# Kernel optimization log

Hardware: AMD Instinct MI355X
Metric: run time of the kernel (lower is better)

## Reference

```python
import jax, jax.numpy as jnp
import numpy as np
from jax import lax

B, S, D, H, FF, STEPS = 8, 1024, 512, 8, 2048, 64
HD = D // H
EPS = 1e-5
NEG_INF = -1e30


def setup_inputs() -> dict:
    key = jax.random.key(0)
    ks = jax.random.split(key, 8)
    sc = 0.02
    inp = {
        "x": jax.random.normal(ks[0], (B, S, D), jnp.float32),
        "decode_x": jax.random.normal(ks[1], (STEPS, B, 1, D), jnp.float32),
        # bool attn mask, True = masked (future positions), matching the torch code
        "causal_mask": jnp.triu(jnp.ones((S, S), bool), k=1),
        "qkv_w": jax.random.normal(ks[2], (3 * D, D), jnp.float32) * sc,
        "qkv_b": jnp.zeros((3 * D,), jnp.float32),
        "out_w": jax.random.normal(ks[3], (D, D), jnp.float32) * sc,
        "out_b": jnp.zeros((D,), jnp.float32),
        "w1": jax.random.normal(ks[4], (FF, D), jnp.float32) * sc,
        "b1": jnp.zeros((FF,), jnp.float32),
        "w2": jax.random.normal(ks[5], (D, FF), jnp.float32) * sc,
        "b2": jnp.zeros((D,), jnp.float32),
        "ln1_w": jnp.ones((D,), jnp.float32),
        "ln1_b": jnp.zeros((D,), jnp.float32),
        "ln2_w": jnp.ones((D,), jnp.float32),
        "ln2_b": jnp.zeros((D,), jnp.float32),
    }
    return inp


def _layer_norm(x, w, b):
    mu = jnp.mean(x, axis=-1, keepdims=True)
    var = jnp.mean(jnp.square(x - mu), axis=-1, keepdims=True)
    return (x - mu) * lax.rsqrt(var + EPS) * w + b


def _mlp(x, w1, b1, w2, b2):
    h = jax.nn.relu(jnp.einsum("bsd,fd->bsf", x, w1) + b1)
    return jnp.einsum("bsf,df->bsd", h, w2) + b2


def _attend(q, k, v, mask):
    # q:[B,H,L,hd] k,v:[B,H,T,hd] mask broadcastable to [B,H,L,T], True = masked
    scale = 1.0 / np.sqrt(HD)
    scores = jnp.einsum("bhld,bhtd->bhlt", q, k) * scale
    scores = jnp.where(mask, NEG_INF, scores)
    w = jax.nn.softmax(scores, axis=-1)
    w = jnp.where(mask, 0.0, w)  # torch code zeros masked weights post-softmax
    return jnp.einsum("bhlt,bhtd->bhld", w, v)


def _heads(t):  # [B,T,D] -> [B,H,T,hd]
    return t.reshape(t.shape[0], t.shape[1], H, HD).transpose(0, 2, 1, 3)


def reference(x, decode_x, causal_mask, qkv_w, qkv_b, out_w, out_b,
              w1, b1, w2, b2, ln1_w, ln1_b, ln2_w, ln2_b):
    # ---- process_prompt (prefill) ----
    qkv = jnp.einsum("bsd,ed->bse", x, qkv_w) + qkv_b  # [B,S,3D]
    q, k, v = jnp.split(qkv, 3, axis=-1)
    attn = _attend(_heads(q), _heads(k), _heads(v), causal_mask[None, None])
    attn = attn.transpose(0, 2, 1, 3).reshape(B, S, D)
    h = x + (jnp.einsum("bsd,ed->bse", attn, out_w) + out_b)
    h = _layer_norm(h, ln1_w, ln1_b)
    h = h + _mlp(h, w1, b1, w2, b2)
    prefill_out = _layer_norm(h, ln2_w, ln2_b)

    cap = S + STEPS
    k_cache = jnp.zeros((B, cap, D), x.dtype).at[:, :S].set(k)
    v_cache = jnp.zeros((B, cap, D), x.dtype).at[:, :S].set(v)
    pos = jnp.arange(cap)

    def step(carry, x_t):
        k_cache, v_cache, cur_len = carry
        qkv = jnp.einsum("bsd,ed->bse", x_t, qkv_w) + qkv_b  # [B,1,3D]
        q, kk, vv = jnp.split(qkv, 3, axis=-1)
        k_cache = lax.dynamic_update_slice(k_cache, kk, (0, cur_len, 0))
        v_cache = lax.dynamic_update_slice(v_cache, vv, (0, cur_len, 0))
        kv_len = cur_len + 1
        mask = (pos >= kv_len)[None, None, None, :]  # [1,1,1,cap]
        attn = _attend(_heads(q), _heads(k_cache), _heads(v_cache), mask)
        attn = attn.transpose(0, 2, 1, 3).reshape(B, 1, D)
        h = x_t + (jnp.einsum("bsd,ed->bse", attn, out_w) + out_b)
        h = _layer_norm(h, ln1_w, ln1_b)
        h = h + _mlp(h, w1, b1, w2, b2)
        h = _layer_norm(h, ln2_w, ln2_b)
        return (k_cache, v_cache, kv_len), h

    (_, _, _), dec = lax.scan(step, (k_cache, v_cache, jnp.int32(S)), decode_x)
    dec = dec.squeeze(2).transpose(1, 0, 2)  # [B,STEPS,D]
    return jnp.concatenate([prefill_out, dec], axis=1)  # [B,S+STEPS,D]
```

## Files before the change

### kernel.cpp

```cpp
#include <hip/hip_runtime.h>
#include <cstdint>

#define CAP_ 1088
#define EPS_ 1e-5f

using bf8   = __attribute__((ext_vector_type(8))) short;
using f32x4 = __attribute__((ext_vector_type(4))) float;

__device__ __forceinline__ unsigned short f2bf(float f) {
  unsigned u = __float_as_uint(f);
  u += 0x7fffu + ((u >> 16) & 1);
  return (unsigned short)(u >> 16);
}
__device__ __forceinline__ float bf2f(unsigned short v) {
  return __uint_as_float((unsigned)v << 16);
}

typedef const __attribute__((address_space(1))) void* gp1;
typedef __attribute__((address_space(3))) void* lp3;
__device__ __forceinline__ void async16(const void* g, void* l) {
  __builtin_amdgcn_global_load_lds((gp1)g, (lp3)l, 16, 0, 0);
}

__global__ __launch_bounds__(256) void cvt_bf16(const float* __restrict__ in,
                                                unsigned short* __restrict__ out,
                                                int n4) {
  int i = blockIdx.x * 256 + threadIdx.x;
  if (i >= n4) return;
  float4 v = ((const float4*)in)[i];
  ushort4 o;
  o.x = f2bf(v.x); o.y = f2bf(v.y); o.z = f2bf(v.z); o.w = f2bf(v.w);
  ((ushort4*)out)[i] = o;
}

__global__ __launch_bounds__(256) void mfma_gemm(
    const unsigned short* __restrict__ A, const unsigned short* __restrict__ Bw,
    const float* __restrict__ bias,
    unsigned short* __restrict__ Cb,
    unsigned short* __restrict__ kb, unsigned short* __restrict__ vt,
    int M, int N, int K, int mode, int relu)
{
  __shared__ unsigned short Als[128 * 64];
  __shared__ unsigned short Bls[128 * 64];
  const int tid  = threadIdx.x;
  const int lane = tid & 63, w = tid >> 6;
  const int bm = blockIdx.x * 128, bn = blockIdx.y * 128;
  const int wm = (w >> 1) * 64, wn = (w & 1) * 64;

  f32x4 acc[4][4] = {};

  const int so = tid * 16;
  for (int k0 = 0; k0 < K; k0 += 64) {
#pragma unroll
    for (int it = 0; it < 4; ++it) {
      int o   = it * 4096 + so;
      int row = o >> 7;
      int ch  = (o >> 4) & 7;
      int sch = ch ^ (row & 7);
      async16(A  + (size_t)(bm + row) * K + k0 + sch * 8, (char*)Als + o);
      async16(Bw + (size_t)(bn + row) * K + k0 + sch * 8, (char*)Bls + o);
    }
    __syncthreads();
#pragma unroll
    for (int ks = 0; ks < 2; ++ks) {
      bf8 af[4], bfr[4];
#pragma unroll
      for (int m = 0; m < 4; ++m) {
        int row = wm + m * 16 + (lane & 15);
        int ch  = ks * 4 + (lane >> 4);
        af[m] = *(const bf8*)((const char*)Als + row * 128 + ((ch ^ (row & 7)) * 16));
      }
#pragma unroll
      for (int n = 0; n < 4; ++n) {
        int row = wn + n * 16 + (lane & 15);
        int ch  = ks * 4 + (lane >> 4);
        bfr[n] = *(const bf8*)((const char*)Bls + row * 128 + ((ch ^ (row & 7)) * 16));
      }
#pragma unroll
      for (int m = 0; m < 4; ++m)
#pragma unroll
        for (int n = 0; n < 4; ++n)
          acc[m][n] = __builtin_amdgcn_mfma_f32_16x16x32_bf16(af[m], bfr[n], acc[m][n], 0, 0, 0);
    }
    __syncthreads();
  }

#pragma unroll
  for (int m = 0; m < 4; ++m) {
#pragma unroll
    for (int n = 0; n < 4; ++n) {
      int col  = bn + wn + n * 16 + (lane & 15);
      int row0 = bm + wm + m * 16 + ((lane >> 4) << 2);
      float bcol = bias[col];
      if (mode == 1) {
        if (col < 512) {
#pragma unroll
          for (int r = 0; r < 4; ++r)
            Cb[((size_t)(row0 + r) << 9) + col] = f2bf((acc[m][n][r] + bcol) * 0.125f);
        } else if (col < 1024) {
#pragma unroll
          for (int r = 0; r < 4; ++r) {
            int row = row0 + r; int bb, pos;
            if (row < 8192) { bb = row >> 10; pos = row & 1023; }
            else { int r2 = row - 8192; bb = r2 & 7; pos = 1024 + (r2 >> 3); }
            kb[(((size_t)(bb * CAP_ + pos)) << 9) + (col - 512)] = f2bf(acc[m][n][r] + bcol);
          }
        } else {
          int c = col - 1024; int hh = c >> 6, d = c & 63;
          if (row0 < 8192) {
            int bb = row0 >> 10, pos = row0 & 1023;
            ushort4 pk;
            pk.x = f2bf(acc[m][n][0] + bcol); pk.y = f2bf(acc[m][n][1] + bcol);
            pk.z = f2bf(acc[m][n][2] + bcol); pk.w = f2bf(acc[m][n][3] + bcol);
            *(ushort4*)(vt + ((size_t)((bb * 8 + hh) * 64 + d)) * CAP_ + pos) = pk;
          } else {
#pragma unroll
            for (int r = 0; r < 4; ++r) {
              int r2 = row0 + r - 8192; int bb = r2 & 7, pos = 1024 + (r2 >> 3);
              vt[((size_t)((bb * 8 + hh) * 64 + d)) * CAP_ + pos] = f2bf(acc[m][n][r] + bcol);
            }
          }
        }
      } else {
#pragma unroll
        for (int r = 0; r < 4; ++r) {
          float v = acc[m][n][r] + bcol;
          if (relu) v = fmaxf(v, 0.f);
          Cb[(size_t)(row0 + r) * N + col] = f2bf(v);
        }
      }
    }
  }
}

__global__ __launch_bounds__(256) void gemm_fullrow_ln(
    const unsigned short* __restrict__ A,
    const unsigned short* __restrict__ Bw,
    const float* __restrict__ bias,
    const unsigned short* __restrict__ resb,
    const float* __restrict__ lnw, const float* __restrict__ lnb,
    unsigned short* __restrict__ outb, float* __restrict__ outf,
    int K, int mode)
{
  __shared__ unsigned short Bls[512 * 64];
  const int tid = threadIdx.x, lane = tid & 63, w = tid >> 6;
  const int l4 = lane >> 4, l15 = lane & 15;
  const int bm = blockIdx.x * 32;

  f32x4 acc[2][8] = {};
  bf8 a_cur[2][2], a_nxt[2][2];

#pragma unroll
  for (int ks = 0; ks < 2; ++ks)
#pragma unroll
    for (int mf = 0; mf < 2; ++mf)
      a_cur[ks][mf] = *(const bf8*)(A + (size_t)(bm + mf * 16 + l15) * K + (ks * 4 + l4) * 8);

  for (int k0 = 0; k0 < K; k0 += 64) {
#pragma unroll
    for (int it = 0; it < 16; ++it) {
      int o   = it * 4096 + tid * 16;
      int row = o >> 7;
      int sch = ((o >> 4) & 7) ^ (row & 7);
      async16(Bw + (size_t)row * K + k0 + sch * 8, (char*)Bls + o);
    }
    if (k0 + 64 < K) {
#pragma unroll
      for (int ks = 0; ks < 2; ++ks)
#pragma unroll
        for (int mf = 0; mf < 2; ++mf)
          a_nxt[ks][mf] = *(const bf8*)(A + (size_t)(bm + mf * 16 + l15) * K +
                                        k0 + 64 + (ks * 4 + l4) * 8);
    }
    __syncthreads();
#pragma unroll
    for (int ks = 0; ks < 2; ++ks) {
      int cb = ks * 4 + l4;
#pragma unroll
      for (int nf = 0; nf < 8; ++nf) {
        int row = w * 128 + nf * 16 + l15;
        bf8 bfv = *(const bf8*)((const char*)Bls + row * 128 + ((cb ^ (row & 7)) << 4));
#pragma unroll
        for (int mf = 0; mf < 2; ++mf)
          acc[mf][nf] = __builtin_amdgcn_mfma_f32_16x16x32_bf16(a_cur[ks][mf], bfv, acc[mf][nf], 0, 0, 0);
      }
    }
#pragma unroll
    for (int ks = 0; ks < 2; ++ks)
#pragma unroll
      for (int mf = 0; mf < 2; ++mf)
        a_cur[ks][mf] = a_nxt[ks][mf];
    __syncthreads();
  }

  float bc[8], lw[8], lb[8];
#pragma unroll
  for (int nf = 0; nf < 8; ++nf) {
    int col = w * 128 + nf * 16 + l15;
    bc[nf] = bias[col]; lw[nf] = lnw[col]; lb[nf] = lnb[col];
  }
#pragma unroll
  for (int nf = 0; nf < 8; ++nf) {
    int col = w * 128 + nf * 16 + l15;
#pragma unroll
    for (int mf = 0; mf < 2; ++mf)
#pragma unroll
      for (int r = 0; r < 4; ++r) {
        int rowg = bm + mf * 16 + l4 * 4 + r;
        acc[mf][nf][r] += bc[nf] + bf2f(resb[(size_t)rowg * 512 + col]);
      }
  }

  float* red = (float*)Bls;
#pragma unroll
  for (int mf = 0; mf < 2; ++mf)
#pragma unroll
    for (int r = 0; r < 4; ++r) {
      float s = 0.f, q = 0.f;
#pragma unroll
      for (int nf = 0; nf < 8; ++nf) { float v = acc[mf][nf][r]; s += v; q += v * v; }
#pragma unroll
      for (int off = 1; off < 16; off <<= 1) {
        s += __shfl_xor(s, off, 64); q += __shfl_xor(q, off, 64);
      }
      if (l15 == 0) {
        int rl = mf * 16 + l4 * 4 + r;
        red[rl * 8 + w * 2]     = s;
        red[rl * 8 + w * 2 + 1] = q;
      }
    }
  __syncthreads();

#pragma unroll
  for (int mf = 0; mf < 2; ++mf)
#pragma unroll
    for (int r = 0; r < 4; ++r) {
      int rl = mf * 16 + l4 * 4 + r;
      float S = red[rl * 8 + 0] + red[rl * 8 + 2] + red[rl * 8 + 4] + red[rl * 8 + 6];
      float Q = red[rl * 8 + 1] + red[rl * 8 + 3] + red[rl * 8 + 5] + red[rl * 8 + 7];
      float mu  = S * (1.f / 512.f);
      float var = Q * (1.f / 512.f) - mu * mu;
      float inv = rsqrtf(var + EPS_);
      int rowg = bm + rl;
      if (mode == 0) {
#pragma unroll
        for (int nf = 0; nf < 8; ++nf) {
          int col = w * 128 + nf * 16 + l15;
          float y = (acc[mf][nf][r] - mu) * inv * lw[nf] + lb[nf];
          outb[(size_t)rowg * 512 + col] = f2bf(y);
        }
      } else {
        int b, s2;
        if (rowg < 8192) { b = rowg >> 10; s2 = rowg & 1023; }
        else { int r2 = rowg - 8192; b = r2 & 7; s2 = 1024 + (r2 >> 3); }
        size_t ob = ((size_t)(b * CAP_ + s2)) << 9;
#pragma unroll
        for (int nf = 0; nf < 8; ++nf) {
          int col = w * 128 + nf * 16 + l15;
          outf[ob + col] = (acc[mf][nf][r] - mu) * inv * lw[nf] + lb[nf];
        }
      }
    }
}

__global__ __launch_bounds__(256) void attn_mfma(
    const unsigned short* __restrict__ qb,
    const unsigned short* __restrict__ kcb,
    const unsigned short* __restrict__ vtb,
    unsigned short* __restrict__ ob)
{
  __shared__ unsigned short Kls[4096];
  __shared__ unsigned short Vls[4096];
  __shared__ unsigned short Pls[4096];
  const int st = blockIdx.x, bh = blockIdx.y;
  const int b = bh >> 3, h = bh & 7;
  const bool dec = (st == 16);
  const int tid = threadIdx.x, lane = tid & 63, w = tid >> 6;
  const int wq = w * 16;
  const int nT = dec ? 17 : st + 1;
  const int qi = wq + (lane & 15);
  const size_t g = dec ? (size_t)(8192 + qi * 8 + b)
                       : (size_t)((b << 10) + st * 64 + qi);

  const bf8 qf0 = *(const bf8*)(qb + (g << 9) + h * 64 +      ((lane >> 4) << 3));
  const bf8 qf1 = *(const bf8*)(qb + (g << 9) + h * 64 + 32 + ((lane >> 4) << 3));

  f32x4 oo[4] = {};
  float m_ = -1e30f, l_ = 0.f;

  const size_t kbase = (((size_t)b * CAP_) << 9) + h * 64;
  const size_t vbase = (size_t)((b * 8 + h) * 64) * CAP_;

  for (int t = 0; t < nT; ++t) {
    const int t0 = t * 64;
    __syncthreads();
#pragma unroll
    for (int it = 0; it < 2; ++it) {
      int o   = it * 4096 + tid * 16;
      int row = o >> 7;
      int sch = ((o >> 4) & 7) ^ (row & 7);
      async16(kcb + kbase + (((size_t)(t0 + row)) << 9) + sch * 8, (char*)Kls + o);
      async16(vtb + vbase + (size_t)row * CAP_ + t0 + sch * 8,     (char*)Vls + o);
    }
    __syncthreads();

    f32x4 sfr[4] = {};
#pragma unroll
    for (int ks = 0; ks < 2; ++ks) {
      int cb = ks * 4 + (lane >> 4);
      bf8 qv = ks ? qf1 : qf0;
#pragma unroll
      for (int f = 0; f < 4; ++f) {
        int row = f * 16 + (lane & 15);
        bf8 kf = *(const bf8*)((const char*)Kls + row * 128 + ((cb ^ (row & 7)) << 4));
        sfr[f] = __builtin_amdgcn_mfma_f32_16x16x32_bf16(kf, qv, sfr[f], 0, 0, 0);
      }
    }
    if (t == nT - 1) {
#pragma unroll
      for (int f = 0; f < 4; ++f)
#pragma unroll
        for (int r = 0; r < 4; ++r) {
          int tr = f * 16 + ((lane >> 4) << 2) + r;
          if (tr > qi) sfr[f][r] = -1e30f;
        }
    }

    float pmax = -1e30f;
#pragma unroll
    for (int f = 0; f < 4; ++f)
#pragma unroll
      for (int r = 0; r < 4; ++r) pmax = fmaxf(pmax, sfr[f][r]);
    pmax = fmaxf(pmax, __shfl_xor(pmax, 16, 64));
    pmax = fmaxf(pmax, __shfl_xor(pmax, 32, 64));
    float mn  = fmaxf(m_, pmax);
    float fsc = __expf(m_ - mn);
    float rs = 0.f;
#pragma unroll
    for (int f = 0; f < 4; ++f)
#pragma unroll
      for (int r = 0; r < 4; ++r) {
        float e = __expf(sfr[f][r] - mn);
        sfr[f][r] = e; rs += e;
      }
    rs += __shfl_xor(rs, 16, 64);
    rs += __shfl_xor(rs, 32, 64);
    l_ = l_ * fsc + rs; m_ = mn;
#pragma unroll
    for (int f = 0; f < 4; ++f) oo[f] *= fsc;

#pragma unroll
    for (int f = 0; f < 4; ++f) {
      ushort4 pk;
      pk.x = f2bf(sfr[f][0]); pk.y = f2bf(sfr[f][1]);
      pk.z = f2bf(sfr[f][2]); pk.w = f2bf(sfr[f][3]);
      int tb   = f * 32 + ((lane >> 4) << 3);
      int addr = qi * 128 + ((((tb >> 4)) ^ (qi & 7)) << 4) + (tb & 15);
      *(ushort4*)((char*)Pls + addr) = pk;
    }
    __syncthreads();

#pragma unroll
    for (int ks = 0; ks < 2; ++ks) {
      int cb = ks * 4 + (lane >> 4);
      bf8 pf = *(const bf8*)((const char*)Pls + qi * 128 + ((cb ^ (qi & 7)) << 4));
#pragma unroll
      for (int f = 0; f < 4; ++f) {
        int row = f * 16 + (lane & 15);
        bf8 vf = *(const bf8*)((const char*)Vls + row * 128 + ((cb ^ (row & 7)) << 4));
        oo[f] = __builtin_amdgcn_mfma_f32_16x16x32_bf16(vf, pf, oo[f], 0, 0, 0);
      }
    }
  }

  const float inv = 1.f / l_;
#pragma unroll
  for (int f = 0; f < 4; ++f) {
    ushort4 pk;
    pk.x = f2bf(oo[f][0] * inv); pk.y = f2bf(oo[f][1] * inv);
    pk.z = f2bf(oo[f][2] * inv); pk.w = f2bf(oo[f][3] * inv);
    int d0 = f * 16 + ((lane >> 4) << 2);
    *(ushort4*)(ob + (g << 9) + h * 64 + d0) = pk;
  }
}

extern "C" void kernel_launch(void* const* d_in, const int* in_sizes, int n_in,
                              void* d_out, int out_size, void* d_ws, size_t ws_size,
                              hipStream_t stream)
{
  const float* x     = (const float*)d_in[0];
  const float* dx    = (const float*)d_in[1];
  const float* qkv_w = (const float*)d_in[3];
  const float* qkv_b = (const float*)d_in[4];
  const float* out_w = (const float*)d_in[5];
  const float* out_b = (const float*)d_in[6];
  const float* w1    = (const float*)d_in[7];
  const float* b1    = (const float*)d_in[8];
  const float* w2    = (const float*)d_in[9];
  const float* b2    = (const float*)d_in[10];
  const float* ln1w  = (const float*)d_in[11];
  const float* ln1b  = (const float*)d_in[12];
  const float* ln2w  = (const float*)d_in[13];
  const float* ln2b  = (const float*)d_in[14];
  float* out = (float*)d_out;

  float* ws = (float*)d_ws;
  size_t o = 0;
  unsigned short* x_bf    = (unsigned short*)(ws + o); o += (size_t)8704 * 256;
  unsigned short* qkvw_bf = (unsigned short*)(ws + o); o += 1536 * 256;
  unsigned short* outw_bf = (unsigned short*)(ws + o); o += 512 * 256;
  unsigned short* w1_bf   = (unsigned short*)(ws + o); o += 2048 * 256;
  unsigned short* w2_bf   = (unsigned short*)(ws + o); o += (size_t)512 * 1024;
  unsigned short* qb_bf   = (unsigned short*)(ws + o); o += (size_t)8704 * 256;
  unsigned short* kcb     = (unsigned short*)(ws + o); o += (size_t)8 * CAP_ * 256;
  unsigned short* vtb     = (unsigned short*)(ws + o); o += (size_t)8 * 512 * CAP_ / 2;
  unsigned short* attn_bf = (unsigned short*)(ws + o); o += (size_t)8704 * 256;
  unsigned short* h1_bf   = (unsigned short*)(ws + o); o += (size_t)8704 * 256;
  unsigned short* hid_bf  = (unsigned short*)(ws + o); o += (size_t)8704 * 1024;

  cvt_bf16<<<dim3(4096), 256, 0, stream>>>(x,  x_bf,                      1048576);
  cvt_bf16<<<dim3(256),  256, 0, stream>>>(dx, x_bf + (size_t)8192 * 512, 65536);
  cvt_bf16<<<dim3(768),  256, 0, stream>>>(qkv_w, qkvw_bf, 196608);
  cvt_bf16<<<dim3(256),  256, 0, stream>>>(out_w, outw_bf, 65536);
  cvt_bf16<<<dim3(1024), 256, 0, stream>>>(w1,    w1_bf,   262144);
  cvt_bf16<<<dim3(1024), 256, 0, stream>>>(w2,    w2_bf,   262144);

  mfma_gemm<<<dim3(68, 12), 256, 0, stream>>>(x_bf, qkvw_bf, qkv_b,
      qb_bf, kcb, vtb, 8704, 1536, 512, 1, 0);
  attn_mfma<<<dim3(17, 64), 256, 0, stream>>>(qb_bf, kcb, vtb, attn_bf);
  gemm_fullrow_ln<<<dim3(272), 256, 0, stream>>>(attn_bf, outw_bf, out_b,
      x_bf, ln1w, ln1b, h1_bf, nullptr, 512, 0);
  mfma_gemm<<<dim3(68, 16), 256, 0, stream>>>(h1_bf, w1_bf, b1,
      hid_bf, nullptr, nullptr, 8704, 2048, 512, 2, 1);
  gemm_fullrow_ln<<<dim3(272), 256, 0, stream>>>(hid_bf, w2_bf, b2,
      h1_bf, ln2w, ln2b, nullptr, out, 2048, 1);
}
```

Before: 310.5 us.

## Double-buffer full-row LN GEMM with 8 waves and fuse conversion launches

```diff
diff --git a/kernel.cpp b/kernel.cpp
--- a/kernel.cpp
+++ b/kernel.cpp
@@ -22,15 +22,27 @@
   __builtin_amdgcn_global_load_lds((gp1)g, (lp3)l, 16, 0, 0);
 }
 
-__global__ __launch_bounds__(256) void cvt_bf16(const float* __restrict__ in,
-                                                unsigned short* __restrict__ out,
-                                                int n4) {
-  int i = blockIdx.x * 256 + threadIdx.x;
-  if (i >= n4) return;
-  float4 v = ((const float4*)in)[i];
+__global__ __launch_bounds__(256) void cvt_all(
+    const float* __restrict__ x, const float* __restrict__ dx,
+    const float* __restrict__ qkvw, const float* __restrict__ outw,
+    const float* __restrict__ w1, const float* __restrict__ w2,
+    unsigned short* __restrict__ x_bf, unsigned short* __restrict__ qkvw_bf,
+    unsigned short* __restrict__ outw_bf, unsigned short* __restrict__ w1_bf,
+    unsigned short* __restrict__ w2_bf)
+{
+  const int bid = blockIdx.x;
+  const float* src; unsigned short* dst; int c;
+  if      (bid < 4096) { src = x;    dst = x_bf;                      c = bid;        }
+  else if (bid < 4352) { src = dx;   dst = x_bf + (size_t)8192 * 512; c = bid - 4096; }
+  else if (bid < 5120) { src = qkvw; dst = qkvw_bf;                   c = bid - 4352; }
+  else if (bid < 5376) { src = outw; dst = outw_bf;                   c = bid - 5120; }
+  else if (bid < 6400) { src = w1;   dst = w1_bf;                     c = bid - 5376; }
+  else                 { src = w2;   dst = w2_bf;                     c = bid - 6400; }
+  const int i = c * 256 + threadIdx.x;
+  float4 v = ((const float4*)src)[i];
   ushort4 o;
   o.x = f2bf(v.x); o.y = f2bf(v.y); o.z = f2bf(v.z); o.w = f2bf(v.w);
-  ((ushort4*)out)[i] = o;
+  ((ushort4*)dst)[i] = o;
 }
 
 __global__ __launch_bounds__(256) void mfma_gemm(
@@ -133,7 +145,7 @@
   }
 }
 
-__global__ __launch_bounds__(256) void gemm_fullrow_ln(
+__global__ __launch_bounds__(512) void gemm_fullrow_ln(
     const unsigned short* __restrict__ A,
     const unsigned short* __restrict__ Bw,
     const float* __restrict__ bias,
@@ -142,66 +154,93 @@
     unsigned short* __restrict__ outb, float* __restrict__ outf,
     int K, int mode)
 {
-  __shared__ unsigned short Bls[512 * 64];
-  const int tid = threadIdx.x, lane = tid & 63, w = tid >> 6;
+  __shared__ unsigned short Bls[2][8][4096];
+  const int tid = threadIdx.x, lane = tid & 63, wc = tid >> 6;
   const int l4 = lane >> 4, l15 = lane & 15;
   const int bm = blockIdx.x * 32;
-
-  f32x4 acc[2][8] = {};
-  bf8 a_cur[2][2], a_nxt[2][2];
-
-#pragma unroll
-  for (int ks = 0; ks < 2; ++ks)
-#pragma unroll
-    for (int mf = 0; mf < 2; ++mf)
-      a_cur[ks][mf] = *(const bf8*)(A + (size_t)(bm + mf * 16 + l15) * K + (ks * 4 + l4) * 8);
-
-  for (int k0 = 0; k0 < K; k0 += 64) {
-#pragma unroll
-    for (int it = 0; it < 16; ++it) {
-      int o   = it * 4096 + tid * 16;
-      int row = o >> 7;
-      int sch = ((o >> 4) & 7) ^ (row & 7);
-      async16(Bw + (size_t)row * K + k0 + sch * 8, (char*)Bls + o);
-    }
-    if (k0 + 64 < K) {
-#pragma unroll
-      for (int ks = 0; ks < 2; ++ks)
-#pragma unroll
-        for (int mf = 0; mf < 2; ++mf)
-          a_nxt[ks][mf] = *(const bf8*)(A + (size_t)(bm + mf * 16 + l15) * K +
-                                        k0 + 64 + (ks * 4 + l4) * 8);
-    }
-    __syncthreads();
-#pragma unroll
-    for (int ks = 0; ks < 2; ++ks) {
-      int cb = ks * 4 + l4;
-#pragma unroll
-      for (int nf = 0; nf < 8; ++nf) {
-        int row = w * 128 + nf * 16 + l15;
-        bf8 bfv = *(const bf8*)((const char*)Bls + row * 128 + ((cb ^ (row & 7)) << 4));
-#pragma unroll
-        for (int mf = 0; mf < 2; ++mf)
-          acc[mf][nf] = __builtin_amdgcn_mfma_f32_16x16x32_bf16(a_cur[ks][mf], bfv, acc[mf][nf], 0, 0, 0);
-      }
-    }
-#pragma unroll
-    for (int ks = 0; ks < 2; ++ks)
-#pragma unroll
-      for (int mf = 0; mf < 2; ++mf)
-        a_cur[ks][mf] = a_nxt[ks][mf];
-    __syncthreads();
-  }
-
-  float bc[8], lw[8], lb[8];
-#pragma unroll
-  for (int nf = 0; nf < 8; ++nf) {
-    int col = w * 128 + nf * 16 + l15;
+  const int NT = K >> 6;
+
+  f32x4 acc[2][4] = {};
+  bf8 a0[2][2], a1[2][2];
+
+#define STAGE(t, buf)                                                        \
+  {                                                                          \
+    const int k0_ = (t) * 64;                                                \
+    char* base_ = (char*)&Bls[(buf)][wc][0];                                 \
+    _Pragma("unroll")                                                        \
+    for (int i_ = 0; i_ < 8; ++i_) {                                         \
+      int loff_ = i_ * 1024 + lane * 16;                                     \
+      int row_  = loff_ >> 7;                                                \
+      int sch_  = ((loff_ >> 4) & 7) ^ (row_ & 7);                           \
+      async16(Bw + (size_t)(wc * 64 + row_) * K + k0_ + sch_ * 8,            \
+              base_ + loff_);                                                \
+    }                                                                        \
+  }
+
+#define LOADA(t, dst)                                                        \
+  {                                                                          \
+    const int k0_ = (t) * 64;                                                \
+    _Pragma("unroll")                                                        \
+    for (int ks_ = 0; ks_ < 2; ++ks_)                                        \
+      _Pragma("unroll")                                                      \
+      for (int mf_ = 0; mf_ < 2; ++mf_)                                      \
+        dst[ks_][mf_] = *(const bf8*)(A + (size_t)(bm + mf_ * 16 + l15) * K  \
+                                      + k0_ + (ks_ * 4 + l4) * 8);           \
+  }
+
+#define COMPUTE(buf, a)                                                      \
+  {                                                                          \
+    const char* base_ = (const char*)&Bls[(buf)][wc][0];                     \
+    _Pragma("unroll")                                                        \
+    for (int ks_ = 0; ks_ < 2; ++ks_) {                                      \
+      _Pragma("unroll")                                                      \
+      for (int nf_ = 0; nf_ < 4; ++nf_) {                                    \
+        int lrow_ = nf_ * 16 + l15;                                          \
+        int c_ = ks_ * 4 + l4;                                               \
+        bf8 bv_ = *(const bf8*)(base_ + lrow_ * 128 +                        \
+                                ((c_ ^ (lrow_ & 7)) << 4));                  \
+        _Pragma("unroll")                                                    \
+        for (int mf_ = 0; mf_ < 2; ++mf_)                                    \
+          acc[mf_][nf_] = __builtin_amdgcn_mfma_f32_16x16x32_bf16(           \
+              a[ks_][mf_], bv_, acc[mf_][nf_], 0, 0, 0);                     \
+      }                                                                      \
+    }                                                                        \
+  }
+
+  STAGE(0, 0); LOADA(0, a0);
+  for (int t = 0; t < NT; t += 2) {
+    if (t + 1 < NT) {
+      STAGE(t + 1, 1); LOADA(t + 1, a1);
+      asm volatile("s_waitcnt vmcnt(12)" ::: "memory");
+    } else {
+      asm volatile("s_waitcnt vmcnt(0)" ::: "memory");
+    }
+    __builtin_amdgcn_sched_barrier(0);
+    COMPUTE(0, a0);
+    if (t + 1 < NT) {
+      if (t + 2 < NT) {
+        STAGE(t + 2, 0); LOADA(t + 2, a0);
+        asm volatile("s_waitcnt vmcnt(12)" ::: "memory");
+      } else {
+        asm volatile("s_waitcnt vmcnt(0)" ::: "memory");
+      }
+      __builtin_amdgcn_sched_barrier(0);
+      COMPUTE(1, a1);
+    }
+  }
+#undef STAGE
+#undef LOADA
+#undef COMPUTE
+
+  float bc[4], lw[4], lb[4];
+#pragma unroll
+  for (int nf = 0; nf < 4; ++nf) {
+    int col = wc * 64 + nf * 16 + l15;
     bc[nf] = bias[col]; lw[nf] = lnw[col]; lb[nf] = lnb[col];
   }
 #pragma unroll
-  for (int nf = 0; nf < 8; ++nf) {
-    int col = w * 128 + nf * 16 + l15;
+  for (int nf = 0; nf < 4; ++nf) {
+    int col = wc * 64 + nf * 16 + l15;
 #pragma unroll
     for (int mf = 0; mf < 2; ++mf)
 #pragma unroll
@@ -211,6 +250,7 @@
       }
   }
 
+  __syncthreads();
   float* red = (float*)Bls;
 #pragma unroll
   for (int mf = 0; mf < 2; ++mf)
@@ -218,15 +258,15 @@
     for (int r = 0; r < 4; ++r) {
       float s = 0.f, q = 0.f;
 #pragma unroll
-      for (int nf = 0; nf < 8; ++nf) { float v = acc[mf][nf][r]; s += v; q += v * v; }
+      for (int nf = 0; nf < 4; ++nf) { float v = acc[mf][nf][r]; s += v; q += v * v; }
 #pragma unroll
       for (int off = 1; off < 16; off <<= 1) {
         s += __shfl_xor(s, off, 64); q += __shfl_xor(q, off, 64);
       }
       if (l15 == 0) {
         int rl = mf * 16 + l4 * 4 + r;
-        red[rl * 8 + w * 2]     = s;
-        red[rl * 8 + w * 2 + 1] = q;
+        red[rl * 16 + wc * 2]     = s;
+        red[rl * 16 + wc * 2 + 1] = q;
       }
     }
   __syncthreads();
@@ -236,16 +276,20 @@
 #pragma unroll
     for (int r = 0; r < 4; ++r) {
       int rl = mf * 16 + l4 * 4 + r;
-      float S = red[rl * 8 + 0] + red[rl * 8 + 2] + red[rl * 8 + 4] + red[rl * 8 + 6];
-      float Q = red[rl * 8 + 1] + red[rl * 8 + 3] + red[rl * 8 + 5] + red[rl * 8 + 7];
+      float S = 0.f, Q = 0.f;
+#pragma unroll
+      for (int wq = 0; wq < 8; ++wq) {
+        S += red[rl * 16 + wq * 2];
+        Q += red[rl * 16 + wq * 2 + 1];
+      }
       float mu  = S * (1.f / 512.f);
       float var = Q * (1.f / 512.f) - mu * mu;
       float inv = rsqrtf(var + EPS_);
       int rowg = bm + rl;
       if (mode == 0) {
 #pragma unroll
-        for (int nf = 0; nf < 8; ++nf) {
-          int col = w * 128 + nf * 16 + l15;
+        for (int nf = 0; nf < 4; ++nf) {
+          int col = wc * 64 + nf * 16 + l15;
           float y = (acc[mf][nf][r] - mu) * inv * lw[nf] + lb[nf];
           outb[(size_t)rowg * 512 + col] = f2bf(y);
         }
@@ -255,8 +299,8 @@
         else { int r2 = rowg - 8192; b = r2 & 7; s2 = 1024 + (r2 >> 3); }
         size_t ob = ((size_t)(b * CAP_ + s2)) << 9;
 #pragma unroll
-        for (int nf = 0; nf < 8; ++nf) {
-          int col = w * 128 + nf * 16 + l15;
+        for (int nf = 0; nf < 4; ++nf) {
+          int col = wc * 64 + nf * 16 + l15;
           outf[ob + col] = (acc[mf][nf][r] - mu) * inv * lw[nf] + lb[nf];
         }
       }
@@ -418,20 +462,16 @@
   unsigned short* h1_bf   = (unsigned short*)(ws + o); o += (size_t)8704 * 256;
   unsigned short* hid_bf  = (unsigned short*)(ws + o); o += (size_t)8704 * 1024;
 
-  cvt_bf16<<<dim3(4096), 256, 0, stream>>>(x,  x_bf,                      1048576);
-  cvt_bf16<<<dim3(256),  256, 0, stream>>>(dx, x_bf + (size_t)8192 * 512, 65536);
-  cvt_bf16<<<dim3(768),  256, 0, stream>>>(qkv_w, qkvw_bf, 196608);
-  cvt_bf16<<<dim3(256),  256, 0, stream>>>(out_w, outw_bf, 65536);
-  cvt_bf16<<<dim3(1024), 256, 0, stream>>>(w1,    w1_bf,   262144);
-  cvt_bf16<<<dim3(1024), 256, 0, stream>>>(w2,    w2_bf,   262144);
+  cvt_all<<<dim3(7424), 256, 0, stream>>>(x, dx, qkv_w, out_w, w1, w2,
+      x_bf, qkvw_bf, outw_bf, w1_bf, w2_bf);
 
   mfma_gemm<<<dim3(68, 12), 256, 0, stream>>>(x_bf, qkvw_bf, qkv_b,
       qb_bf, kcb, vtb, 8704, 1536, 512, 1, 0);
   attn_mfma<<<dim3(17, 64), 256, 0, stream>>>(qb_bf, kcb, vtb, attn_bf);
-  gemm_fullrow_ln<<<dim3(272), 256, 0, stream>>>(attn_bf, outw_bf, out_b,
+  gemm_fullrow_ln<<<dim3(272), 512, 0, stream>>>(attn_bf, outw_bf, out_b,
       x_bf, ln1w, ln1b, h1_bf, nullptr, 512, 0);
   mfma_gemm<<<dim3(68, 16), 256, 0, stream>>>(h1_bf, w1_bf, b1,
       hid_bf, nullptr, nullptr, 8704, 2048, 512, 2, 1);
-  gemm_fullrow_ln<<<dim3(272), 256, 0, stream>>>(hid_bf, w2_bf, b2,
+  gemm_fullrow_ln<<<dim3(272), 512, 0, stream>>>(hid_bf, w2_bf, b2,
       h1_bf, ln2w, ln2b, nullptr, out, 2048, 1);
 }
```

New measurement: 334.6 us. 7.8% more time.
